# Optimization experiments

Measured on AMD Instinct MI355X. Metric: run time of the kernel, lower is better.

The kernel has to match this reference:

```python
import jax, jax.numpy as jnp
import numpy as np

N_NODES = 50000
N_EDGES = 800000
N_GRAPHS = 64
NUM_CLASSES = 10


def _glorot(key, shape):
    fan_in, fan_out = shape
    lim = np.sqrt(6.0 / (fan_in + fan_out)).astype(np.float32)
    return jax.random.uniform(key, shape, jnp.float32, -lim, lim)


def setup_inputs() -> dict:
    key = jax.random.key(0)
    ks = jax.random.split(key, 12)
    x = jax.random.normal(ks[0], (N_NODES, 5), jnp.float32)
    edge_index = jax.random.randint(ks[1], (2, N_EDGES), 0, N_NODES, jnp.int64)
    batch = jnp.sort(jax.random.randint(ks[2], (N_NODES,), 0, N_GRAPHS, jnp.int64))
    dims = [5, 32, 64, 128, 256]
    params = {}
    for i in range(4):
        params[f"W{i+1}"] = _glorot(ks[3 + i], (dims[i], dims[i + 1]))
        params[f"b{i+1}"] = jnp.zeros((dims[i + 1],), jnp.float32)
    params["fcW"] = _glorot(ks[7], (256, NUM_CLASSES))
    params["fcb"] = jnp.zeros((NUM_CLASSES,), jnp.float32)
    return {"x": x, "edge_index": edge_index, "batch": batch, **params}


def reference(x, edge_index, batch, W1, b1, W2, b2, W3, b3, W4, b4, fcW, fcb):
    n = x.shape[0]
    loop = jnp.arange(n, dtype=edge_index.dtype)
    src = jnp.concatenate([edge_index[0], loop])  # source nodes (+ self loops)
    dst = jnp.concatenate([edge_index[1], loop])  # target nodes (+ self loops)
    # symmetric GCN normalization: D^{-1/2} (A+I) D^{-1/2}
    deg = jax.ops.segment_sum(jnp.ones_like(dst, x.dtype), dst, num_segments=n)
    dinv = jax.lax.rsqrt(deg)  # deg >= 1 due to self loops
    norm = (dinv[src] * dinv[dst])[:, None]

    def gcn(h, W, b):
        h = h @ W                                        # dense transform
        agg = jax.ops.segment_sum(h[src] * norm, dst, num_segments=n)
        return agg + b

    h = jax.nn.relu(gcn(x, W1, b1))
    h = jax.nn.relu(gcn(h, W2, b2))
    h = jax.nn.relu(gcn(h, W3, b3))
    h = jax.nn.relu(gcn(h, W4, b4))                      # [n, 256]

    # global mean pool over graphs
    counts = jax.ops.segment_sum(jnp.ones((n,), h.dtype), batch, num_segments=N_GRAPHS)
    pooled = jax.ops.segment_sum(h, batch, num_segments=N_GRAPHS)
    pooled = pooled / jnp.maximum(counts, 1.0)[:, None]  # [G, 256]

    return jax.nn.log_softmax(pooled @ fcW + fcb, axis=-1)
```

## Files before the change

kernel.cpp:

```cpp
#include <hip/hip_runtime.h>
#include <hip/hip_bf16.h>
#include <math.h>

#define N_NODES 50000
#define N_EDGES 800000
#define N_GRAPHS 64
#define NUM_CLASSES 10
#define BIN_W 256
#define NBINS ((N_NODES + BIN_W - 1) / BIN_W)
#define CHUNK 4096
#define NCHUNKS ((N_EDGES + CHUNK - 1) / CHUNK)
#define CAP 8192
#define CPB 64
#define PACK_BLOCKS 21

typedef __attribute__((ext_vector_type(8))) short bf16x8;
typedef __attribute__((ext_vector_type(4))) float f32x4;

__device__ inline unsigned short f2bf(float f) {
    unsigned int u = __float_as_uint(f);
    u += 0x7fffu + ((u >> 16) & 1u);
    return (unsigned short)(u >> 16);
}
__device__ inline float bf2f(unsigned short v) {
    return __uint_as_float((unsigned int)v << 16);
}
__device__ inline void bf8_unpack(uint4 v, float* o) {
    o[0] = __uint_as_float(v.x << 16); o[1] = __uint_as_float(v.x & 0xffff0000u);
    o[2] = __uint_as_float(v.y << 16); o[3] = __uint_as_float(v.y & 0xffff0000u);
    o[4] = __uint_as_float(v.z << 16); o[5] = __uint_as_float(v.z & 0xffff0000u);
    o[6] = __uint_as_float(v.w << 16); o[7] = __uint_as_float(v.w & 0xffff0000u);
}
__device__ inline unsigned int pack2(float a, float b) {
    return (unsigned int)f2bf(a) | ((unsigned int)f2bf(b) << 16);
}

template<int K, int N>
__device__ void packW_dev(const float* __restrict__ W, unsigned short* __restrict__ Wp,
                          int bid, int l) {
    constexpr int KT = K / 32;
    int kt = bid % KT, nt = bid / KT;
    int m = l & 15, quad = l >> 4;
    #pragma unroll
    for (int j = 0; j < 8; j++) {
        int k = kt * 32 + quad * 8 + j;
        int n = nt * 16 + m;
        Wp[((size_t)bid * 64 + l) * 8 + j] = f2bf(W[(size_t)k * N + n]);
    }
}

__global__ __launch_bounds__(256) void k_binscatter(const int* __restrict__ src,
                                                    const int* __restrict__ dst,
                                                    unsigned short* __restrict__ cnt,
                                                    unsigned int* __restrict__ binned,
                                                    const float* __restrict__ W2,
                                                    const float* __restrict__ W3,
                                                    const float* __restrict__ W4,
                                                    unsigned short* wp2, unsigned short* wp3,
                                                    unsigned short* wp4) {
    int bid = blockIdx.x, t = threadIdx.x;
    if (bid >= NCHUNKS) {
        int w = (bid - NCHUNKS) * 4 + (t >> 6);
        int lane = t & 63;
        if (w < 4)       packW_dev<32, 64>(W2, wp2, w, lane);
        else if (w < 20) packW_dev<64, 128>(W3, wp3, w - 4, lane);
        else if (w < 84) packW_dev<128, 256>(W4, wp4, w - 20, lane);
        return;
    }
    __shared__ int hist[NBINS];
    __shared__ int off[NBINS];
    __shared__ int bump[NBINS];
    __shared__ unsigned int stage[CHUNK];
    __shared__ unsigned char sbin[CHUNK];
    int base = bid * CHUNK;
    int total = N_EDGES - base; if (total > CHUNK) total = CHUNK;
    for (int i = t; i < NBINS; i += 256) { hist[i] = 0; bump[i] = 0; }
    __syncthreads();
    int es[16], ed[16];
    #pragma unroll
    for (int i = 0; i < 16; i++) {
        int e = base + t + i * 256;
        if (e < N_EDGES) { es[i] = src[e]; ed[i] = dst[e]; }
        else ed[i] = -1;
    }
    #pragma unroll
    for (int i = 0; i < 16; i++)
        if (ed[i] >= 0) atomicAdd(&hist[ed[i] >> 8], 1);
    __syncthreads();
    {
        __shared__ int s[256];
        int v = (t < NBINS) ? hist[t] : 0;
        s[t] = v; __syncthreads();
        for (int o = 1; o < 256; o <<= 1) {
            int x = (t >= o) ? s[t - o] : 0;
            __syncthreads();
            s[t] += x;
            __syncthreads();
        }
        if (t < NBINS) off[t] = s[t] - v;
    }
    __syncthreads();
    #pragma unroll
    for (int i = 0; i < 16; i++) {
        if (ed[i] >= 0) {
            int b = ed[i] >> 8;
            int lpos = off[b] + atomicAdd(&bump[b], 1);
            stage[lpos] = ((unsigned int)(ed[i] & 255) << 16) | (unsigned int)es[i];
            sbin[lpos] = (unsigned char)b;
        }
    }
    __syncthreads();
    for (int j = t; j < total; j += 256) {
        int b = sbin[j];
        int pos = j - off[b];
        if (pos < CPB)
            binned[((size_t)b * NCHUNKS + bid) * CPB + pos] = stage[j];
    }
    if (t < NBINS) {
        int h = hist[t]; if (h > CPB) h = CPB;
        cnt[(size_t)bid * NBINS + t] = (unsigned short)h;
    }
}

__global__ __launch_bounds__(256) void k_csr(const unsigned int* __restrict__ binned,
                                             const unsigned short* __restrict__ cnt,
                                             unsigned int* __restrict__ row_ptr,
                                             float* __restrict__ dinv,
                                             unsigned short* __restrict__ csr16,
                                             const float* __restrict__ x,
                                             float* __restrict__ x5) {
    __shared__ unsigned int stage[CAP];
    __shared__ int coff[256];
    __shared__ int deg[BIN_W];
    __shared__ int off[BIN_W];
    __shared__ int bump[BIN_W];
    __shared__ int s_total;
    int b = blockIdx.x;
    int t = threadIdx.x;
    deg[t] = 0; bump[t] = 0;
    int myc = (t < NCHUNKS) ? (int)cnt[(size_t)t * NBINS + b] : 0;
    {
        __shared__ int s[256];
        s[t] = myc; __syncthreads();
        for (int o = 1; o < 256; o <<= 1) {
            int v = (t >= o) ? s[t - o] : 0;
            __syncthreads();
            s[t] += v;
            __syncthreads();
        }
        coff[t] = s[t] - myc;
        if (t == 255) s_total = s[255];
    }
    __syncthreads();
    int total = s_total; if (total > CAP) total = CAP;
    if (t < NCHUNKS && myc > 0) {
        const unsigned int* seg = &binned[((size_t)b * NCHUNKS + t) * CPB];
        int o0 = coff[t];
        for (int j = 0; j < myc && o0 + j < CAP; j++)
            stage[o0 + j] = seg[j];
    }
    __syncthreads();
    for (int e = t; e < total; e += 256)
        atomicAdd(&deg[stage[e] >> 16], 1);
    __syncthreads();
    {
        __shared__ int s[256];
        int v = deg[t];
        s[t] = v; __syncthreads();
        for (int o = 1; o < 256; o <<= 1) {
            int x2 = (t >= o) ? s[t - o] : 0;
            __syncthreads();
            s[t] += x2;
            __syncthreads();
        }
        off[t] = s[t] - v;
    }
    __syncthreads();
    int e0 = b * CAP;
    int node = b * BIN_W + t;
    if (node < N_NODES) {
        float di = rsqrtf((float)(deg[t] + 1));
        row_ptr[node] = (unsigned int)(e0 + off[t]) | ((unsigned int)deg[t] << 21);
        dinv[node] = di;
        #pragma unroll
        for (int f = 0; f < 5; f++)
            x5[node * 5 + f] = di * x[node * 5 + f];
    }
    for (int e = t; e < total; e += 256) {
        unsigned int v = stage[e];
        int dl = v >> 16;
        int pos = e0 + off[dl] + atomicAdd(&bump[dl], 1);
        csr16[pos] = (unsigned short)(v & 0xffffu);
    }
}

__global__ __launch_bounds__(256) void k_layer1(const float* __restrict__ x5,
                                                const unsigned int* __restrict__ row_ptr,
                                                const unsigned short* __restrict__ csr16,
                                                const float* __restrict__ dinv,
                                                const float* __restrict__ W1,
                                                const float* __restrict__ b1,
                                                unsigned short* __restrict__ Hout) {
    __shared__ float A5[32 * 6];
    __shared__ float Ws[160];
    __shared__ float bs[32];
    int t = threadIdx.x;
    int row0 = blockIdx.x * 32;
    if (t < 160) Ws[t] = W1[t];
    if (t >= 224) bs[t - 224] = b1[t - 224];
    int nl = t >> 3, f = t & 7;
    int node = row0 + nl;
    float val = 0.0f;
    float dnode = 0.0f;
    if (node < N_NODES) dnode = dinv[node];
    if (f < 5 && node < N_NODES) {
        float acc0 = x5[node * 5 + f], acc1 = 0.0f;
        unsigned int v = row_ptr[node];
        int e0 = (int)(v & 0x1FFFFFu);
        int e1 = e0 + (int)(v >> 21);
        int e = e0;
        for (; e + 7 < e1; e += 8) {
            int s0 = csr16[e], s1 = csr16[e + 1], s2 = csr16[e + 2], s3 = csr16[e + 3];
            int s4 = csr16[e + 4], s5 = csr16[e + 5], s6 = csr16[e + 6], s7 = csr16[e + 7];
            float x0 = x5[s0 * 5 + f], x1 = x5[s1 * 5 + f];
            float x2 = x5[s2 * 5 + f], x3 = x5[s3 * 5 + f];
            float x4 = x5[s4 * 5 + f], x5v = x5[s5 * 5 + f];
            float x6 = x5[s6 * 5 + f], x7 = x5[s7 * 5 + f];
            acc0 += (x0 + x2) + (x4 + x6);
            acc1 += (x1 + x3) + (x5v + x7);
        }
        for (; e + 3 < e1; e += 4) {
            int s0 = csr16[e], s1 = csr16[e + 1], s2 = csr16[e + 2], s3 = csr16[e + 3];
            float x0 = x5[s0 * 5 + f], x1 = x5[s1 * 5 + f];
            float x2 = x5[s2 * 5 + f], x3 = x5[s3 * 5 + f];
            acc0 += x0 + x2;
            acc1 += x1 + x3;
        }
        for (; e < e1; e++) acc0 += x5[csr16[e] * 5 + f];
        val = dnode * (acc0 + acc1);
    }
    if (f < 5) A5[nl * 6 + f] = val;
    __syncthreads();
    int j0 = (t & 7) * 4;
    int node2 = row0 + (t >> 3);
    float d2 = (node2 < N_NODES) ? dinv[node2] : 0.0f;
    float a[5];
    #pragma unroll
    for (int k = 0; k < 5; k++) a[k] = A5[(t >> 3) * 6 + k];
    ushort4 o;
    unsigned short* op = (unsigned short*)&o;
    #pragma unroll
    for (int c = 0; c < 4; c++) {
        float acc = bs[j0 + c];
        #pragma unroll
        for (int k = 0; k < 5; k++) acc += a[k] * Ws[k * 32 + j0 + c];
        op[c] = f2bf(d2 * fmaxf(acc, 0.0f));
    }
    if (node2 < N_NODES) *(ushort4*)&Hout[(size_t)node2 * 32 + j0] = o;
}

template<int K, int N, bool SCALE, bool POOL>
__global__ __launch_bounds__(256) void k_fused(const unsigned short* __restrict__ Hin,
                                               const unsigned int* __restrict__ row_ptr,
                                               const unsigned short* __restrict__ csr16,
                                               const float* __restrict__ dinv,
                                               const unsigned short* __restrict__ Wp,
                                               const float* __restrict__ bias,
                                               unsigned short* __restrict__ C,
                                               const int* __restrict__ batch,
                                               float* __restrict__ pooled) {
    constexpr int KT = K / 32, NT = N / 16, DV = K / 8;
    constexpr int NPB = 2048 / K;
    constexpr int TM = NPB / 16;
    constexpr int KP = K + 8;
    __shared__ unsigned short As[NPB * KP];
    __shared__ int bb[POOL ? NPB : 4];
    int t = threadIdx.x;
    int row0 = blockIdx.x * NPB;
    if constexpr (POOL) {
        if (t < NPB) bb[t] = batch[min(row0 + t, N_NODES - 1)];
    }
    {
        int nl = t / DV, f = t % DV;
        int node = row0 + nl;
        const uint4* h4 = (const uint4*)Hin;
        uint4 o = {0u, 0u, 0u, 0u};
        if (node < N_NODES) {
            float di = dinv[node];
            float acc0[8], acc1[8];
            bf8_unpack(h4[(size_t)node * DV + f], acc0);
            #pragma unroll
            for (int i = 0; i < 8; i++) acc1[i] = 0.0f;
            unsigned int rv = row_ptr[node];
            int e0 = (int)(rv & 0x1FFFFFu);
            int e1 = e0 + (int)(rv >> 21);
            int e = e0;
            for (; e + 3 < e1; e += 4) {
                int s0 = csr16[e], s1 = csr16[e + 1], s2 = csr16[e + 2], s3 = csr16[e + 3];
                uint4 u0 = h4[(size_t)s0 * DV + f];
                uint4 u1 = h4[(size_t)s1 * DV + f];
                uint4 u2 = h4[(size_t)s2 * DV + f];
                uint4 u3 = h4[(size_t)s3 * DV + f];
                float t0[8], t1[8], t2[8], t3[8];
                bf8_unpack(u0, t0); bf8_unpack(u1, t1);
                bf8_unpack(u2, t2); bf8_unpack(u3, t3);
                #pragma unroll
                for (int i = 0; i < 8; i++) {
                    acc0[i] += t0[i] + t2[i];
                    acc1[i] += t1[i] + t3[i];
                }
            }
            for (; e + 1 < e1; e += 2) {
                int s0 = csr16[e], s1 = csr16[e + 1];
                uint4 u0 = h4[(size_t)s0 * DV + f];
                uint4 u1 = h4[(size_t)s1 * DV + f];
                float t0[8], t1[8];
                bf8_unpack(u0, t0);
                bf8_unpack(u1, t1);
                #pragma unroll
                for (int i = 0; i < 8; i++) { acc0[i] += t0[i]; acc1[i] += t1[i]; }
            }
            if (e < e1) {
                float t0[8];
                bf8_unpack(h4[(size_t)csr16[e] * DV + f], t0);
                #pragma unroll
                for (int i = 0; i < 8; i++) acc0[i] += t0[i];
            }
            o.x = pack2(di * (acc0[0] + acc1[0]), di * (acc0[1] + acc1[1]));
            o.y = pack2(di * (acc0[2] + acc1[2]), di * (acc0[3] + acc1[3]));
            o.z = pack2(di * (acc0[4] + acc1[4]), di * (acc0[5] + acc1[5]));
            o.w = pack2(di * (acc0[6] + acc1[6]), di * (acc0[7] + acc1[7]));
        }
        *(uint4*)&As[nl * KP + f * 8] = o;
    }
    __syncthreads();
    int wave = t >> 6, lane = t & 63;
    int m = lane & 15, quad = lane >> 4;
    bf16x8 a[TM][KT];
    float dr[TM][4];
    #pragma unroll
    for (int mt = 0; mt < TM; mt++) {
        #pragma unroll
        for (int kt = 0; kt < KT; kt++)
            a[mt][kt] = *(const bf16x8*)&As[(mt * 16 + m) * KP + kt * 32 + quad * 8];
        #pragma unroll
        for (int r = 0; r < 4; r++) {
            int row = row0 + mt * 16 + quad * 4 + r;
            dr[mt][r] = (SCALE && row < N_NODES) ? dinv[row] : 1.0f;
        }
    }
    const bf16x8* Bp = (const bf16x8*)Wp;
    int g0 = 0, g1 = 0;
    if constexpr (POOL) { g0 = bb[0]; g1 = bb[NPB - 1]; }
    for (int j = wave; j < TM * NT; j += 4) {
        int mt = j % TM, nt = j / TM;
        f32x4 c = {0.f, 0.f, 0.f, 0.f};
        #pragma unroll
        for (int kt = 0; kt < KT; kt++)
            c = __builtin_amdgcn_mfma_f32_16x16x32_bf16(a[mt][kt],
                    Bp[(size_t)(nt * KT + kt) * 64 + lane], c, 0, 0, 0);
        int col = nt * 16 + m;
        float bv = bias[col];
        if constexpr (POOL) {
            float acc0 = 0.0f, acc1 = 0.0f;
            #pragma unroll
            for (int r = 0; r < 4; r++) {
                int rl = mt * 16 + quad * 4 + r;
                int row = row0 + rl;
                if (row < N_NODES) {
                    float v = fmaxf(c[r] + bv, 0.0f);
                    int g = bb[rl];
                    if (g == g0) acc0 += v;
                    else if (g == g1) acc1 += v;
                    else atomicAdd(&pooled[(size_t)g * 256 + col], v);
                }
            }
            acc0 += __shfl_xor(acc0, 32); acc0 += __shfl_xor(acc0, 16);
            acc1 += __shfl_xor(acc1, 32); acc1 += __shfl_xor(acc1, 16);
            if (lane < 16) {
                atomicAdd(&pooled[(size_t)g0 * 256 + col], acc0);
                if (g1 != g0) atomicAdd(&pooled[(size_t)g1 * 256 + col], acc1);
            }
        } else {
            #pragma unroll
            for (int r = 0; r < 4; r++) {
                int row = row0 + mt * 16 + quad * 4 + r;
                if (row < N_NODES) {
                    float v = fmaxf(c[r] + bv, 0.0f);
                    if constexpr (SCALE) v *= dr[mt][r];
                    C[(size_t)row * N + col] = f2bf(v);
                }
            }
        }
    }
}

__global__ void k_final(const float* __restrict__ pooled, const int* __restrict__ batch,
                        const float* __restrict__ fcW, const float* __restrict__ fcb,
                        float* __restrict__ out) {
    int g = blockIdx.x;
    int t = threadIdx.x;
    float cnt = 0.0f;
    if (t == 0) {
        int lo = 0, hi = N_NODES;
        while (lo < hi) { int m = (lo + hi) >> 1; if (batch[m] < g) lo = m + 1; else hi = m; }
        int start = lo;
        lo = 0; hi = N_NODES;
        while (lo < hi) { int m = (lo + hi) >> 1; if (batch[m] < g + 1) lo = m + 1; else hi = m; }
        cnt = (float)(lo - start);
    }
    float inv = 1.0f / fmaxf(__shfl(cnt, 0), 1.0f);
    float p[4];
    #pragma unroll
    for (int m = 0; m < 4; m++) p[m] = pooled[g * 256 + t + 64 * m];
    float logits[NUM_CLASSES];
    #pragma unroll
    for (int j = 0; j < NUM_CLASSES; j++) {
        float s = 0.0f;
        #pragma unroll
        for (int m = 0; m < 4; m++) s += p[m] * fcW[(t + 64 * m) * NUM_CLASSES + j];
        for (int off = 32; off > 0; off >>= 1) s += __shfl_xor(s, off);
        logits[j] = s * inv + fcb[j];
    }
    float mx = logits[0];
    #pragma unroll
    for (int j = 1; j < NUM_CLASSES; j++) mx = fmaxf(mx, logits[j]);
    float se = 0.0f;
    #pragma unroll
    for (int j = 0; j < NUM_CLASSES; j++) se += expf(logits[j] - mx);
    float lse = mx + logf(se);
    if (t < NUM_CLASSES) out[g * NUM_CLASSES + t] = logits[t] - lse;
}

extern "C" void kernel_launch(void* const* d_in, const int* in_sizes, int n_in,
                              void* d_out, int out_size, void* d_ws, size_t ws_size,
                              hipStream_t stream) {
    const float* x     = (const float*)d_in[0];
    const int*   ei    = (const int*)d_in[1];
    const int*   src   = ei;
    const int*   dst   = ei + N_EDGES;
    const int*   batch = (const int*)d_in[2];
    const float* W1 = (const float*)d_in[3];  const float* b1 = (const float*)d_in[4];
    const float* W2 = (const float*)d_in[5];  const float* b2 = (const float*)d_in[6];
    const float* W3 = (const float*)d_in[7];  const float* b3 = (const float*)d_in[8];
    const float* W4 = (const float*)d_in[9];  const float* b4 = (const float*)d_in[10];
    const float* fcW = (const float*)d_in[11]; const float* fcb = (const float*)d_in[12];
    float* out = (float*)d_out;

    char* ws = (char*)d_ws;
    unsigned short* buf1 = (unsigned short*)ws; ws += (size_t)N_NODES * 256 * 2;
    unsigned short* buf2 = (unsigned short*)ws; ws += (size_t)N_NODES * 256 * 2;
    float* dinv     = (float*)ws; ws += (size_t)N_NODES * 4;
    float* x5       = (float*)ws; ws += (size_t)N_NODES * 5 * 4 + 16;
    unsigned int* row_ptr = (unsigned int*)ws; ws += (size_t)(N_NODES + 4) * 4;
    unsigned short* csr16 = (unsigned short*)ws; ws += (size_t)NBINS * CAP * 2;
    unsigned int* binned = (unsigned int*)ws; ws += (size_t)NBINS * NCHUNKS * CPB * 4;
    unsigned short* cnt = (unsigned short*)ws; ws += (size_t)NCHUNKS * NBINS * 2 + 16;
    float* pooled   = (float*)ws; ws += (size_t)N_GRAPHS * 256 * 4;
    unsigned short* wp2 = (unsigned short*)ws; ws += 32 * 64 * 2;
    unsigned short* wp3 = (unsigned short*)ws; ws += 64 * 128 * 2;
    unsigned short* wp4 = (unsigned short*)ws; ws += 128 * 256 * 2;

    const int TB = 256;
    k_binscatter<<<NCHUNKS + PACK_BLOCKS, TB, 0, stream>>>(src, dst, cnt, binned,
                                                           W2, W3, W4, wp2, wp3, wp4);
    k_csr<<<NBINS, TB, 0, stream>>>(binned, cnt, row_ptr, dinv, csr16, x, x5);

    k_layer1<<<(N_NODES + 31) / 32, TB, 0, stream>>>(x5, row_ptr, csr16, dinv, W1, b1, buf1);
    k_fused<32, 64, true, false><<<(N_NODES + 63) / 64, TB, 0, stream>>>(
        buf1, row_ptr, csr16, dinv, wp2, b2, buf2, nullptr, nullptr);
    k_fused<64, 128, true, false><<<(N_NODES + 31) / 32, TB, 0, stream>>>(
        buf2, row_ptr, csr16, dinv, wp3, b3, buf1, nullptr, nullptr);
    k_fused<128, 256, false, true><<<(N_NODES + 15) / 16, TB, 0, stream>>>(
        buf1, row_ptr, csr16, dinv, wp4, b4, nullptr, batch, pooled);

    k_final<<<N_GRAPHS, 64, 0, stream>>>(pooled, batch, fcW, fcb, out);
}
```

Baseline: 194.3 us.

## Merge per-layer kernels into one persistent cooperative kernel with grid syncs

Replaces the four layer launches and the final pooling/softmax launch with a single cooperative persistent kernel. Blocks loop over work units, and grid.sync() separates the layers. This removes per-launch overhead and the tail idle time between kernels. In exchange it adds grid-wide barrier costs, caps occupancy through a shared 6 KB smem buffer and launch bounds of 8 blocks, and drops the 8-way unrolled edge loop in layer 1.

```diff
diff --git a/kernel.cpp b/kernel.cpp
--- a/kernel.cpp
+++ b/kernel.cpp
@@ -1,6 +1,9 @@
 #include <hip/hip_runtime.h>
 #include <hip/hip_bf16.h>
+#include <hip/hip_cooperative_groups.h>
 #include <math.h>
+
+namespace cg = cooperative_groups;
 
 #define N_NODES 50000
 #define N_EDGES 800000
@@ -13,6 +16,7 @@
 #define CAP 8192
 #define CPB 64
 #define PACK_BLOCKS 21
+#define SMEM_BYTES 6144
 
 typedef __attribute__((ext_vector_type(8))) short bf16x8;
 typedef __attribute__((ext_vector_type(4))) float f32x4;
@@ -21,9 +25,6 @@
     unsigned int u = __float_as_uint(f);
     u += 0x7fffu + ((u >> 16) & 1u);
     return (unsigned short)(u >> 16);
-}
-__device__ inline float bf2f(unsigned short v) {
-    return __uint_as_float((unsigned int)v << 16);
 }
 __device__ inline void bf8_unpack(uint4 v, float* o) {
     o[0] = __uint_as_float(v.x << 16); o[1] = __uint_as_float(v.x & 0xffff0000u);
@@ -194,41 +195,29 @@
     }
 }
 
-__global__ __launch_bounds__(256) void k_layer1(const float* __restrict__ x5,
-                                                const unsigned int* __restrict__ row_ptr,
-                                                const unsigned short* __restrict__ csr16,
-                                                const float* __restrict__ dinv,
-                                                const float* __restrict__ W1,
-                                                const float* __restrict__ b1,
-                                                unsigned short* __restrict__ Hout) {
-    __shared__ float A5[32 * 6];
-    __shared__ float Ws[160];
-    __shared__ float bs[32];
+__device__ void layer1_body(char* smem, int u, const float* __restrict__ x5,
+                            const unsigned int* __restrict__ row_ptr,
+                            const unsigned short* __restrict__ csr16,
+                            const float* __restrict__ dinv,
+                            const float* __restrict__ W1, const float* __restrict__ b1,
+                            unsigned short* __restrict__ Hout) {
+    float* A5 = (float*)smem;
+    float* Ws = A5 + 192;
+    float* bs = Ws + 160;
     int t = threadIdx.x;
-    int row0 = blockIdx.x * 32;
+    int row0 = u * 32;
     if (t < 160) Ws[t] = W1[t];
     if (t >= 224) bs[t - 224] = b1[t - 224];
     int nl = t >> 3, f = t & 7;
     int node = row0 + nl;
     float val = 0.0f;
-    float dnode = 0.0f;
-    if (node < N_NODES) dnode = dinv[node];
     if (f < 5 && node < N_NODES) {
+        float dnode = dinv[node];
         float acc0 = x5[node * 5 + f], acc1 = 0.0f;
         unsigned int v = row_ptr[node];
         int e0 = (int)(v & 0x1FFFFFu);
         int e1 = e0 + (int)(v >> 21);
         int e = e0;
-        for (; e + 7 < e1; e += 8) {
-            int s0 = csr16[e], s1 = csr16[e + 1], s2 = csr16[e + 2], s3 = csr16[e + 3];
-            int s4 = csr16[e + 4], s5 = csr16[e + 5], s6 = csr16[e + 6], s7 = csr16[e + 7];
-            float x0 = x5[s0 * 5 + f], x1 = x5[s1 * 5 + f];
-            float x2 = x5[s2 * 5 + f], x3 = x5[s3 * 5 + f];
-            float x4 = x5[s4 * 5 + f], x5v = x5[s5 * 5 + f];
-            float x6 = x5[s6 * 5 + f], x7 = x5[s7 * 5 + f];
-            acc0 += (x0 + x2) + (x4 + x6);
-            acc1 += (x1 + x3) + (x5v + x7);
-        }
         for (; e + 3 < e1; e += 4) {
             int s0 = csr16[e], s1 = csr16[e + 1], s2 = csr16[e + 2], s3 = csr16[e + 3];
             float x0 = x5[s0 * 5 + f], x1 = x5[s1 * 5 + f];
@@ -257,26 +246,27 @@
         op[c] = f2bf(d2 * fmaxf(acc, 0.0f));
     }
     if (node2 < N_NODES) *(ushort4*)&Hout[(size_t)node2 * 32 + j0] = o;
+    __syncthreads();
 }
 
 template<int K, int N, bool SCALE, bool POOL>
-__global__ __launch_bounds__(256) void k_fused(const unsigned short* __restrict__ Hin,
-                                               const unsigned int* __restrict__ row_ptr,
-                                               const unsigned short* __restrict__ csr16,
-                                               const float* __restrict__ dinv,
-                                               const unsigned short* __restrict__ Wp,
-                                               const float* __restrict__ bias,
-                                               unsigned short* __restrict__ C,
-                                               const int* __restrict__ batch,
-                                               float* __restrict__ pooled) {
+__device__ void fused_body(char* smem, int u, const unsigned short* __restrict__ Hin,
+                           const unsigned int* __restrict__ row_ptr,
+                           const unsigned short* __restrict__ csr16,
+                           const float* __restrict__ dinv,
+                           const unsigned short* __restrict__ Wp,
+                           const float* __restrict__ bias,
+                           unsigned short* __restrict__ C,
+                           const int* __restrict__ batch,
+                           float* __restrict__ pooled) {
     constexpr int KT = K / 32, NT = N / 16, DV = K / 8;
     constexpr int NPB = 2048 / K;
     constexpr int TM = NPB / 16;
     constexpr int KP = K + 8;
-    __shared__ unsigned short As[NPB * KP];
-    __shared__ int bb[POOL ? NPB : 4];
+    unsigned short* As = (unsigned short*)smem;
+    int* bb = (int*)(smem + NPB * KP * 2);
     int t = threadIdx.x;
-    int row0 = blockIdx.x * NPB;
+    int row0 = u * NPB;
     if constexpr (POOL) {
         if (t < NPB) bb[t] = batch[min(row0 + t, N_NODES - 1)];
     }
@@ -393,15 +383,16 @@
             }
         }
     }
-}
-
-__global__ void k_final(const float* __restrict__ pooled, const int* __restrict__ batch,
-                        const float* __restrict__ fcW, const float* __restrict__ fcb,
-                        float* __restrict__ out) {
-    int g = blockIdx.x;
-    int t = threadIdx.x;
+    __syncthreads();
+}
+
+__device__ void final_body(int g, const float* __restrict__ pooled,
+                           const int* __restrict__ batch,
+                           const float* __restrict__ fcW, const float* __restrict__ fcb,
+                           float* __restrict__ out) {
+    int lane = threadIdx.x & 63;
     float cnt = 0.0f;
-    if (t == 0) {
+    if (lane == 0) {
         int lo = 0, hi = N_NODES;
         while (lo < hi) { int m = (lo + hi) >> 1; if (batch[m] < g) lo = m + 1; else hi = m; }
         int start = lo;
@@ -412,13 +403,13 @@
     float inv = 1.0f / fmaxf(__shfl(cnt, 0), 1.0f);
     float p[4];
     #pragma unroll
-    for (int m = 0; m < 4; m++) p[m] = pooled[g * 256 + t + 64 * m];
+    for (int m = 0; m < 4; m++) p[m] = pooled[g * 256 + lane + 64 * m];
     float logits[NUM_CLASSES];
     #pragma unroll
     for (int j = 0; j < NUM_CLASSES; j++) {
         float s = 0.0f;
         #pragma unroll
-        for (int m = 0; m < 4; m++) s += p[m] * fcW[(t + 64 * m) * NUM_CLASSES + j];
+        for (int m = 0; m < 4; m++) s += p[m] * fcW[(lane + 64 * m) * NUM_CLASSES + j];
         for (int off = 32; off > 0; off >>= 1) s += __shfl_xor(s, off);
         logits[j] = s * inv + fcb[j];
     }
@@ -429,7 +420,50 @@
     #pragma unroll
     for (int j = 0; j < NUM_CLASSES; j++) se += expf(logits[j] - mx);
     float lse = mx + logf(se);
-    if (t < NUM_CLASSES) out[g * NUM_CLASSES + t] = logits[t] - lse;
+    if (lane < NUM_CLASSES) out[g * NUM_CLASSES + lane] = logits[lane] - lse;
+}
+
+__global__ __launch_bounds__(256, 8) void k_net(const float* __restrict__ x5,
+                                                const unsigned int* __restrict__ row_ptr,
+                                                const unsigned short* __restrict__ csr16,
+                                                const float* __restrict__ dinv,
+                                                const float* __restrict__ W1,
+                                                const float* __restrict__ b1,
+                                                const unsigned short* __restrict__ wp2,
+                                                const float* __restrict__ b2,
+                                                const unsigned short* __restrict__ wp3,
+                                                const float* __restrict__ b3,
+                                                const unsigned short* __restrict__ wp4,
+                                                const float* __restrict__ b4,
+                                                unsigned short* __restrict__ buf1,
+                                                unsigned short* __restrict__ buf2,
+                                                const int* __restrict__ batch,
+                                                float* __restrict__ pooled,
+                                                const float* __restrict__ fcW,
+                                                const float* __restrict__ fcb,
+                                                float* __restrict__ out) {
+    cg::grid_group grid = cg::this_grid();
+    __shared__ __align__(16) char smem[SMEM_BYTES];
+    const int G = gridDim.x;
+
+    for (int u = blockIdx.x; u < (N_NODES + 31) / 32; u += G)
+        layer1_body(smem, u, x5, row_ptr, csr16, dinv, W1, b1, buf1);
+    grid.sync();
+    for (int u = blockIdx.x; u < (N_NODES + 63) / 64; u += G)
+        fused_body<32, 64, true, false>(smem, u, buf1, row_ptr, csr16, dinv, wp2, b2,
+                                        buf2, nullptr, nullptr);
+    grid.sync();
+    for (int u = blockIdx.x; u < (N_NODES + 31) / 32; u += G)
+        fused_body<64, 128, true, false>(smem, u, buf2, row_ptr, csr16, dinv, wp3, b3,
+                                         buf1, nullptr, nullptr);
+    grid.sync();
+    for (int u = blockIdx.x; u < (N_NODES + 15) / 16; u += G)
+        fused_body<128, 256, false, true>(smem, u, buf1, row_ptr, csr16, dinv, wp4, b4,
+                                          nullptr, batch, pooled);
+    grid.sync();
+    int wave = threadIdx.x >> 6;
+    for (int g = blockIdx.x * 4 + wave; g < N_GRAPHS; g += G * 4)
+        final_body(g, pooled, batch, fcW, fcb, out);
 }
 
 extern "C" void kernel_launch(void* const* d_in, const int* in_sizes, int n_in,
@@ -466,13 +500,16 @@
                                                            W2, W3, W4, wp2, wp3, wp4);
     k_csr<<<NBINS, TB, 0, stream>>>(binned, cnt, row_ptr, dinv, csr16, x, x5);
 
-    k_layer1<<<(N_NODES + 31) / 32, TB, 0, stream>>>(x5, row_ptr, csr16, dinv, W1, b1, buf1);
-    k_fused<32, 64, true, false><<<(N_NODES + 63) / 64, TB, 0, stream>>>(
-        buf1, row_ptr, csr16, dinv, wp2, b2, buf2, nullptr, nullptr);
-    k_fused<64, 128, true, false><<<(N_NODES + 31) / 32, TB, 0, stream>>>(
-        buf2, row_ptr, csr16, dinv, wp3, b3, buf1, nullptr, nullptr);
-    k_fused<128, 256, false, true><<<(N_NODES + 15) / 16, TB, 0, stream>>>(
-        buf1, row_ptr, csr16, dinv, wp4, b4, nullptr, batch, pooled);
-
-    k_final<<<N_GRAPHS, 64, 0, stream>>>(pooled, batch, fcW, fcb, out);
-}
+    int maxb = 0;
+    hipOccupancyMaxActiveBlocksPerMultiprocessor(&maxb, k_net, TB, 0);
+    if (maxb < 1) maxb = 4;
+    int grid = maxb * 256;
+    if (grid > 2048) grid = 2048;
+    void* kargs[] = {
+        (void*)&x5, (void*)&row_ptr, (void*)&csr16, (void*)&dinv,
+        (void*)&W1, (void*)&b1, (void*)&wp2, (void*)&b2, (void*)&wp3, (void*)&b3,
+        (void*)&wp4, (void*)&b4, (void*)&buf1, (void*)&buf2, (void*)&batch,
+        (void*)&pooled, (void*)&fcW, (void*)&fcb, (void*)&out
+    };
+    hipLaunchCooperativeKernel((const void*)k_net, dim3(grid), dim3(TB), kargs, 0, stream);
+}
```

Measured after the change: 734.9 us. 278% more time.
